# Performance work log

Measured on AMD Instinct MI355X. Metric: run time of the kernel, lower is better.

Reference implementation:

```python
import jax, jax.numpy as jnp
import numpy as np

N = 50000      # nodes
E = 800000     # edges
F_IN = 128     # input_dim
H = 4          # GAT heads
C = 32         # hidden_dim (per head)
HC = H * C     # 128, concat GAT output
NG = 64        # graphs in batch
OUT = 10       # classes


def _gat_conv(x, src, dst, W, att_src, att_dst, bias):
    # PyG GATConv (concat=True, add_self_loops=True, negative_slope=0.2)
    n = x.shape[0]
    h = (x @ W).reshape(n, H, -1)                      # [N,H,C]
    a_s = (h * att_src).sum(-1)                        # [N,H]
    a_d = (h * att_dst).sum(-1)                        # [N,H]
    loop = jnp.arange(n)
    s = jnp.concatenate([src, loop])                   # self-loops appended
    d = jnp.concatenate([dst, loop])
    e = jax.nn.leaky_relu(a_s[s] + a_d[d], 0.2)        # [E+N,H]
    m = jax.ops.segment_max(e, d, num_segments=n)
    e = jnp.exp(e - m[d])
    z = jax.ops.segment_sum(e, d, num_segments=n)
    alpha = e / (z[d] + 1e-16)                         # edge softmax per dst,head
    out = jax.ops.segment_sum(h[s] * alpha[..., None], d, num_segments=n)
    return out.reshape(n, -1) + bias                   # [N,H*C]


def setup_inputs() -> dict:
    key = jax.random.key(0)
    ks = jax.random.split(key, 20)
    g = lambda k, shp, fan: jax.random.normal(k, shp, jnp.float32) / np.sqrt(fan)
    inp = {
        'x': jax.random.normal(ks[0], (N, F_IN), jnp.float32),
        'edge_index': jax.random.randint(ks[1], (2, E), 0, N),
        'batch': jnp.sort(jax.random.randint(ks[2], (N,), 0, NG)),
        # GATConv 1: F_IN -> H*C
        'W1': g(ks[3], (F_IN, HC), F_IN),
        'as1': g(ks[4], (H, C), C), 'ad1': g(ks[5], (H, C), C),
        'b1': jnp.zeros((HC,), jnp.float32),
        # GATConv 2: H*C -> H*C
        'W2': g(ks[6], (HC, HC), HC),
        'as2': g(ks[7], (H, C), C), 'ad2': g(ks[8], (H, C), C),
        'b2': jnp.zeros((HC,), jnp.float32),
        # GraphConv: H*C -> C  (lin_rel has bias, lin_root does not)
        'W3r': g(ks[9], (HC, C), HC), 'W3l': g(ks[10], (HC, C), HC),
        'b3': jnp.zeros((C,), jnp.float32),
        # SAGEConv: C -> C (mean aggr; lin_l has bias, lin_r does not)
        'W4l': g(ks[11], (C, C), C), 'b4l': jnp.zeros((C,), jnp.float32),
        'W4r': g(ks[12], (C, C), C),
        # MLP head
        'Wf1': g(ks[13], (C, C), C), 'bf1': jnp.zeros((C,), jnp.float32),
        'Wf2': g(ks[14], (C, OUT), C), 'bf2': jnp.zeros((OUT,), jnp.float32),
    }
    return inp


def reference(x, edge_index, batch, W1, as1, ad1, b1, W2, as2, ad2, b2,
              W3r, W3l, b3, W4l, b4l, W4r, Wf1, bf1, Wf2, bf2):
    src, dst = edge_index[0], edge_index[1]
    relu = jax.nn.relu
    n = x.shape[0]
    # GAT layers (dropout is identity in eval)
    x = relu(_gat_conv(x, src, dst, W1, as1, ad1, b1))
    x = relu(_gat_conv(x, src, dst, W2, as2, ad2, b2))
    # GraphConv: lin_rel(sum_neighbors) + lin_root(x)
    agg = jax.ops.segment_sum(x[src], dst, num_segments=n)
    x = relu(agg @ W3r + b3 + x @ W3l)
    # SAGEConv: lin_l(mean_neighbors) + lin_r(x)
    deg = jax.ops.segment_sum(jnp.ones((src.shape[0],), x.dtype), dst, num_segments=n)
    mean = jax.ops.segment_sum(x[src], dst, num_segments=n) / jnp.maximum(deg, 1.0)[:, None]
    x = relu(mean @ W4l + b4l + x @ W4r)
    # global mean pool over graphs
    cnt = jax.ops.segment_sum(jnp.ones((n,), x.dtype), batch, num_segments=NG)
    gpool = jax.ops.segment_sum(x, batch, num_segments=NG) / jnp.maximum(cnt, 1.0)[:, None]
    gpool = relu(gpool @ Wf1 + bf1)
    return gpool @ Wf2 + bf2
```

## Files before the change

kernel.cpp:

```cpp
#include <hip/hip_runtime.h>
#include <hip/hip_bf16.h>
#include <type_traits>


typedef __bf16 v8bf __attribute__((ext_vector_type(8)));
typedef float  v4f  __attribute__((ext_vector_type(4)));

__device__ __forceinline__ float lrelu(float x) { return x > 0.f ? x : 0.2f * x; }

__device__ __forceinline__ float bf2f(__hip_bfloat16 b) {
    unsigned short u = *(const unsigned short*)&b;
    return __uint_as_float((unsigned)u << 16);
}
__device__ __forceinline__ unsigned short f2bf(float f) {
    unsigned u = __float_as_uint(f);
    unsigned r = (u + 0x7FFF + ((u >> 16) & 1)) >> 16;
    return (unsigned short)r;
}
__device__ __forceinline__ float bflo(int v) { return __uint_as_float((unsigned)v << 16); }
__device__ __forceinline__ float bfhi(int v) { return __uint_as_float((unsigned)v & 0xffff0000u); }
__device__ __forceinline__ int packbf2(float a, float b) {
    return (int)f2bf(a) | ((int)f2bf(b) << 16);
}


__global__ __launch_bounds__(256) void bucket_hist(const int* __restrict__ dst,
                                                   int* __restrict__ bcount,
                                                   int E, int nbuck) {
    __shared__ int hist[256];
    int t = threadIdx.x;
    for (int i = t; i < nbuck; i += 256) hist[i] = 0;
    __syncthreads();
    int base = blockIdx.x * 4096;
    #pragma unroll
    for (int k = 0; k < 16; ++k) {
        int e = base + k * 256 + t;
        if (e < E) atomicAdd(&hist[dst[e] >> 8], 1);
    }
    __syncthreads();
    for (int i = t; i < nbuck; i += 256) {
        int c = hist[i];
        if (c) atomicAdd(&bcount[i], c);
    }
}

__global__ __launch_bounds__(256) void scan_buckets(const int* __restrict__ bcount,
                                                    int* __restrict__ bbase,
                                                    int* __restrict__ gcursor,
                                                    int nbuck, int E,
                                                    int* __restrict__ rowptr, int n) {
    __shared__ int red[256];
    int t = threadIdx.x;
    int v = (t < nbuck) ? bcount[t] : 0;
    red[t] = v;
    __syncthreads();
    for (int off = 1; off < 256; off <<= 1) {
        int u = (t >= off) ? red[t - off] : 0;
        __syncthreads();
        red[t] += u;
        __syncthreads();
    }
    int ex = red[t] - v;
    if (t < nbuck) { bbase[t] = ex; gcursor[t] = ex; }
    if (t == 0) { bbase[nbuck] = E; rowptr[n] = E; }
}

__global__ __launch_bounds__(256) void bucket_scatter(const int* __restrict__ dst,
                                                      const int* __restrict__ src,
                                                      int* __restrict__ gcursor,
                                                      int* __restrict__ pairs,
                                                      int E, int nbuck) {
    __shared__ int hist[256], lcur[256];
    int t = threadIdx.x;
    for (int i = t; i < nbuck; i += 256) hist[i] = 0;
    __syncthreads();
    int base = blockIdx.x * 2048;
    int dreg[8];
    #pragma unroll
    for (int k = 0; k < 8; ++k) {
        int e = base + k * 256 + t;
        int d = (e < E) ? dst[e] : -1;
        dreg[k] = d;
        if (d >= 0) atomicAdd(&hist[d >> 8], 1);
    }
    __syncthreads();
    for (int i = t; i < nbuck; i += 256) {
        int c = hist[i];
        lcur[i] = c ? atomicAdd(&gcursor[i], c) : 0;
    }
    __syncthreads();
    #pragma unroll
    for (int k = 0; k < 8; ++k) {
        int e = base + k * 256 + t;
        if (e < E) {
            int d = dreg[k];
            int p = atomicAdd(&lcur[d >> 8], 1);
            pairs[p] = ((d & 255) << 17) | src[e];
        }
    }
}

__global__ __launch_bounds__(256) void bucket_fill(const int* __restrict__ pairs,
                                                   const int* __restrict__ bbase,
                                                   int* __restrict__ rowptr,
                                                   int* __restrict__ colsrc, int n) {
    __shared__ int deg[256], excl[256], cur[256];
    int b = blockIdx.x, t = threadIdx.x;
    int e0 = bbase[b], e1 = bbase[b + 1];
    int d0 = b << 8;
    deg[t] = 0;
    __syncthreads();
    for (int j = e0 + t; j < e1; j += 256)
        atomicAdd(&deg[pairs[j] >> 17], 1);
    __syncthreads();
    int v = deg[t];
    excl[t] = v;
    __syncthreads();
    for (int off = 1; off < 256; off <<= 1) {
        int u = (t >= off) ? excl[t - off] : 0;
        __syncthreads();
        excl[t] += u;
        __syncthreads();
    }
    int base = e0 + excl[t] - v;
    if (d0 + t < n) rowptr[d0 + t] = base;
    cur[t] = base;
    __syncthreads();
    for (int j = e0 + t; j < e1; j += 256) {
        int w = pairs[j];
        int p = atomicAdd(&cur[w >> 17], 1);
        colsrc[p] = w & 0x1FFFF;
    }
}

__global__ void convert_weights(const float* __restrict__ W1, const float* __restrict__ W2,
                                const float* __restrict__ W3r, const float* __restrict__ W3l,
                                __hip_bfloat16* __restrict__ W1t, __hip_bfloat16* __restrict__ W2t,
                                __hip_bfloat16* __restrict__ W3rt, __hip_bfloat16* __restrict__ W3lt) {
    int i = blockIdx.x * 256 + threadIdx.x;
    if (i < 16384) {
        int k = i >> 7, c = i & 127;
        *(unsigned short*)&W1t[c * 128 + k] = f2bf(W1[i]);
        *(unsigned short*)&W2t[c * 128 + k] = f2bf(W2[i]);
    }
    if (i < 4096) {
        int k = i >> 5, c = i & 31;
        *(unsigned short*)&W3rt[c * 128 + k] = f2bf(W3r[i]);
        *(unsigned short*)&W3lt[c * 128 + k] = f2bf(W3l[i]);
    }
}

template <typename T>
__global__ __launch_bounds__(256) void gemm_att_mfma(
    const T* __restrict__ X, const __hip_bfloat16* __restrict__ Wt,
    const float* __restrict__ att_s, const float* __restrict__ att_d,
    __hip_bfloat16* __restrict__ h, float* __restrict__ a_s, float* __restrict__ a_d, int n)
{
    __shared__ __align__(16) __hip_bfloat16 sWt[128 * 136];
    int t = threadIdx.x;
    for (int i = t; i < 128 * 16; i += 256) {
        int row = i >> 4, ch = i & 15;
        *(int4*)&sWt[row * 136 + ch * 8] = *(const int4*)&Wt[row * 128 + ch * 8];
    }
    __syncthreads();
    int wave = t >> 6, lane = t & 63, quad = lane >> 4, l16 = lane & 15;
    int rowbase = (blockIdx.x * 4 + wave) * 16;
    if (rowbase >= n) return;

    v8bf z;
    #pragma unroll
    for (int i = 0; i < 8; ++i) z[i] = (__bf16)0.f;
    int arow = rowbase + l16;
    bool ok = arow < n;
    v8bf af[4];
    if constexpr (std::is_same<T, float>::value) {
        const float* xf = X + (size_t)(ok ? arow : 0) * 128;
        #pragma unroll
        for (int ks = 0; ks < 4; ++ks) {
            if (ok) {
                float4 u = *(const float4*)&xf[ks * 32 + quad * 8];
                float4 v = *(const float4*)&xf[ks * 32 + quad * 8 + 4];
                v8bf a;
                unsigned short r;
                r = f2bf(u.x); a[0] = *(__bf16*)&r;
                r = f2bf(u.y); a[1] = *(__bf16*)&r;
                r = f2bf(u.z); a[2] = *(__bf16*)&r;
                r = f2bf(u.w); a[3] = *(__bf16*)&r;
                r = f2bf(v.x); a[4] = *(__bf16*)&r;
                r = f2bf(v.y); a[5] = *(__bf16*)&r;
                r = f2bf(v.z); a[6] = *(__bf16*)&r;
                r = f2bf(v.w); a[7] = *(__bf16*)&r;
                af[ks] = a;
            } else af[ks] = z;
        }
    } else {
        const v8bf* px = (const v8bf*)(X + (size_t)(ok ? arow : 0) * 128);
        #pragma unroll
        for (int ks = 0; ks < 4; ++ks) af[ks] = ok ? px[ks * 4 + quad] : z;
    }

    v4f acc[8];
    #pragma unroll
    for (int ct = 0; ct < 8; ++ct) acc[ct] = (v4f){0.f, 0.f, 0.f, 0.f};
    #pragma unroll
    for (int ct = 0; ct < 8; ++ct) {
        #pragma unroll
        for (int ks = 0; ks < 4; ++ks) {
            v8bf b = *(const v8bf*)&sWt[(ct * 16 + l16) * 136 + ks * 32 + quad * 8];
            acc[ct] = __builtin_amdgcn_mfma_f32_16x16x32_bf16(af[ks], b, acc[ct], 0, 0, 0);
        }
    }

    float sas[4][4], sad[4][4];
    #pragma unroll
    for (int r = 0; r < 4; ++r)
        #pragma unroll
        for (int hd = 0; hd < 4; ++hd) { sas[r][hd] = 0.f; sad[r][hd] = 0.f; }
    #pragma unroll
    for (int ct = 0; ct < 8; ++ct) {
        float sa = att_s[ct * 16 + l16];
        float da = att_d[ct * 16 + l16];
        int hd = ct >> 1;
        #pragma unroll
        for (int r = 0; r < 4; ++r) {
            float v = acc[ct][r];
            sas[r][hd] += v * sa;
            sad[r][hd] += v * da;
        }
    }
    #pragma unroll
    for (int reg = 0; reg < 4; ++reg) {
        int r = rowbase + quad * 4 + reg;
        if (r < n) {
            #pragma unroll
            for (int ct = 0; ct < 8; ++ct)
                *(unsigned short*)&h[(size_t)r * 128 + ct * 16 + l16] = f2bf(acc[ct][reg]);
        }
    }
    #pragma unroll
    for (int off = 1; off < 16; off <<= 1) {
        #pragma unroll
        for (int r = 0; r < 4; ++r)
            #pragma unroll
            for (int hd = 0; hd < 4; ++hd) {
                sas[r][hd] += __shfl_xor(sas[r][hd], off);
                sad[r][hd] += __shfl_xor(sad[r][hd], off);
            }
    }
    if (l16 == 0) {
        #pragma unroll
        for (int reg = 0; reg < 4; ++reg) {
            int r = rowbase + quad * 4 + reg;
            if (r < n) {
                float4 vs = {sas[reg][0], sas[reg][1], sas[reg][2], sas[reg][3]};
                float4 vd = {sad[reg][0], sad[reg][1], sad[reg][2], sad[reg][3]};
                *(float4*)&a_s[r * 4] = vs;
                *(float4*)&a_d[r * 4] = vd;
            }
        }
    }
}

__global__ __launch_bounds__(256) void gat_aggr(
    const __hip_bfloat16* __restrict__ h, const float* __restrict__ a_s,
    const float* __restrict__ a_d,
    const int* __restrict__ rowptr, const int* __restrict__ colsrc,
    const float* __restrict__ bias, __hip_bfloat16* __restrict__ out, int n)
{
    __shared__ float s_w[4][64 * 4];
    int t = threadIdx.x;
    int wave = t >> 6, lane = t & 63;
    int d = blockIdx.x * 4 + wave;
    if (d >= n) d = n - 1;
    int beg = rowptr[d], end = rowptr[d + 1];
    int cnt = end - beg;
    float4 ad4 = *(const float4*)&a_d[d * 4];
    float4 asd = *(const float4*)&a_s[d * 4];
    float es0 = lrelu(asd.x + ad4.x), es1 = lrelu(asd.y + ad4.y);
    float es2 = lrelu(asd.z + ad4.z), es3 = lrelu(asd.w + ad4.w);
    float z0 = 0.f, z1 = 0.f, z2 = 0.f, z3 = 0.f;

    int l16 = lane & 15, egrp = lane >> 4;
    int ch = l16 * 8;
    int head = l16 >> 2;
    float acc[8];
    #pragma unroll
    for (int i = 0; i < 8; ++i) acc[i] = 0.f;

    for (int j0 = 0; j0 < cnt; j0 += 64) {
        int ne = min(64, cnt - j0);
        float w0 = 0.f, w1 = 0.f, w2 = 0.f, w3 = 0.f;
        int s = 0;
        if (lane < ne) {
            s = colsrc[beg + j0 + lane];
            float4 sv = *(const float4*)&a_s[s * 4];
            w0 = __expf(lrelu(sv.x + ad4.x));
            w1 = __expf(lrelu(sv.y + ad4.y));
            w2 = __expf(lrelu(sv.z + ad4.z));
            w3 = __expf(lrelu(sv.w + ad4.w));
        }
        z0 += w0; z1 += w1; z2 += w2; z3 += w3;
        float4 wv = {w0, w1, w2, w3};
        *(float4*)&s_w[wave][lane * 4] = wv;
        __asm volatile("s_waitcnt lgkmcnt(0)" ::: "memory");
        int kmax = (ne + 3) >> 2;
        for (int k = 0; k < kmax; ++k) {
            int j = egrp + 4 * k;
            int ss = __shfl(s, min(j, 63));
            if (j < ne) {
                float wj = s_w[wave][j * 4 + head];
                int4 u = *(const int4*)&h[(size_t)ss * 128 + ch];
                acc[0] += wj * bflo(u.x); acc[1] += wj * bfhi(u.x);
                acc[2] += wj * bflo(u.y); acc[3] += wj * bfhi(u.y);
                acc[4] += wj * bflo(u.z); acc[5] += wj * bfhi(u.z);
                acc[6] += wj * bflo(u.w); acc[7] += wj * bfhi(u.w);
            }
        }
    }
    #pragma unroll
    for (int off = 1; off < 64; off <<= 1) {
        z0 += __shfl_xor(z0, off);
        z1 += __shfl_xor(z1, off);
        z2 += __shfl_xor(z2, off);
        z3 += __shfl_xor(z3, off);
    }
    #pragma unroll
    for (int off = 16; off < 64; off <<= 1)
        #pragma unroll
        for (int i = 0; i < 8; ++i) acc[i] += __shfl_xor(acc[i], off);

    if (egrp == 0) {
        float zh = (head < 2) ? (head == 0 ? z0 : z1) : (head == 2 ? z2 : z3);
        float eh = (head < 2) ? (head == 0 ? es0 : es1) : (head == 2 ? es2 : es3);
        float ws = __expf(eh);
        float inv = 1.f / (zh + ws + 1e-16f);
        int4 hu = *(const int4*)&h[(size_t)d * 128 + ch];
        float hs[8] = {bflo(hu.x), bfhi(hu.x), bflo(hu.y), bfhi(hu.y),
                       bflo(hu.z), bfhi(hu.z), bflo(hu.w), bfhi(hu.w)};
        float4 b0 = *(const float4*)&bias[ch];
        float4 b1 = *(const float4*)&bias[ch + 4];
        float o[8];
        o[0] = fmaxf((acc[0] + ws * hs[0]) * inv + b0.x, 0.f);
        o[1] = fmaxf((acc[1] + ws * hs[1]) * inv + b0.y, 0.f);
        o[2] = fmaxf((acc[2] + ws * hs[2]) * inv + b0.z, 0.f);
        o[3] = fmaxf((acc[3] + ws * hs[3]) * inv + b0.w, 0.f);
        o[4] = fmaxf((acc[4] + ws * hs[4]) * inv + b1.x, 0.f);
        o[5] = fmaxf((acc[5] + ws * hs[5]) * inv + b1.y, 0.f);
        o[6] = fmaxf((acc[6] + ws * hs[6]) * inv + b1.z, 0.f);
        o[7] = fmaxf((acc[7] + ws * hs[7]) * inv + b1.w, 0.f);
        int4 ou;
        ou.x = packbf2(o[0], o[1]); ou.y = packbf2(o[2], o[3]);
        ou.z = packbf2(o[4], o[5]); ou.w = packbf2(o[6], o[7]);
        *(int4*)&out[(size_t)d * 128 + ch] = ou;
    }
}

__global__ __launch_bounds__(256) void graphconv_lin(
    const __hip_bfloat16* __restrict__ Xb,
    const __hip_bfloat16* __restrict__ Wrt, const __hip_bfloat16* __restrict__ Wlt,
    const float* __restrict__ bias, __hip_bfloat16* __restrict__ y,
    float* __restrict__ root, int n)
{
    __shared__ __align__(16) __hip_bfloat16 sWr[32 * 136], sWl[32 * 136];
    int t = threadIdx.x;
    for (int i = t; i < 32 * 16; i += 256) {
        int row = i >> 4, ch = i & 15;
        *(int4*)&sWr[row * 136 + ch * 8] = *(const int4*)&Wrt[row * 128 + ch * 8];
        *(int4*)&sWl[row * 136 + ch * 8] = *(const int4*)&Wlt[row * 128 + ch * 8];
    }
    __syncthreads();
    int wave = t >> 6, lane = t & 63, quad = lane >> 4, l16 = lane & 15;
    int rowbase = (blockIdx.x * 4 + wave) * 16;
    if (rowbase >= n) return;

    v8bf z;
    #pragma unroll
    for (int i = 0; i < 8; ++i) z[i] = (__bf16)0.f;
    int arow = rowbase + l16;
    bool ok = arow < n;
    const v8bf* px = (const v8bf*)(Xb + (size_t)(ok ? arow : 0) * 128);
    v8bf fx[4];
    #pragma unroll
    for (int ks = 0; ks < 4; ++ks) fx[ks] = ok ? px[ks * 4 + quad] : z;

    v4f accR[2], accL[2];
    #pragma unroll
    for (int ct = 0; ct < 2; ++ct) {
        accR[ct] = (v4f){0.f, 0.f, 0.f, 0.f};
        accL[ct] = (v4f){0.f, 0.f, 0.f, 0.f};
        #pragma unroll
        for (int ks = 0; ks < 4; ++ks) {
            v8bf br = *(const v8bf*)&sWr[(ct * 16 + l16) * 136 + ks * 32 + quad * 8];
            accR[ct] = __builtin_amdgcn_mfma_f32_16x16x32_bf16(fx[ks], br, accR[ct], 0, 0, 0);
            v8bf bl = *(const v8bf*)&sWl[(ct * 16 + l16) * 136 + ks * 32 + quad * 8];
            accL[ct] = __builtin_amdgcn_mfma_f32_16x16x32_bf16(fx[ks], bl, accL[ct], 0, 0, 0);
        }
    }
    #pragma unroll
    for (int ct = 0; ct < 2; ++ct) {
        float bcol = bias[ct * 16 + l16];
        #pragma unroll
        for (int reg = 0; reg < 4; ++reg) {
            int r = rowbase + quad * 4 + reg;
            if (r < n) {
                *(unsigned short*)&y[(size_t)r * 32 + ct * 16 + l16] = f2bf(accR[ct][reg]);
                root[(size_t)r * 32 + ct * 16 + l16] = accL[ct][reg] + bcol;
            }
        }
    }
}

__global__ __launch_bounds__(256) void graphconv_aggr(
    const __hip_bfloat16* __restrict__ y, const float* __restrict__ root,
    const int* __restrict__ rowptr, const int* __restrict__ colsrc,
    __hip_bfloat16* __restrict__ x3, int n)
{
    int t = threadIdx.x;
    int wave = t >> 6, lane = t & 63;
    int d = blockIdx.x * 4 + wave;
    if (d >= n) d = n - 1;
    int beg = rowptr[d], end = rowptr[d + 1];
    int cnt = end - beg;
    int l4 = lane & 3, egrp = lane >> 2;
    int ch = l4 * 8;
    float acc[8];
    #pragma unroll
    for (int i = 0; i < 8; ++i) acc[i] = 0.f;
    for (int j0 = 0; j0 < cnt; j0 += 64) {
        int ne = min(64, cnt - j0);
        int s = (lane < ne) ? colsrc[beg + j0 + lane] : 0;
        int kmax = (ne + 15) >> 4;
        for (int k = 0; k < kmax; ++k) {
            int j = egrp + 16 * k;
            int ss = __shfl(s, min(j, 63));
            if (j < ne) {
                int4 u = *(const int4*)&y[(size_t)ss * 32 + ch];
                acc[0] += bflo(u.x); acc[1] += bfhi(u.x);
                acc[2] += bflo(u.y); acc[3] += bfhi(u.y);
                acc[4] += bflo(u.z); acc[5] += bfhi(u.z);
                acc[6] += bflo(u.w); acc[7] += bfhi(u.w);
            }
        }
    }
    #pragma unroll
    for (int off = 4; off < 64; off <<= 1)
        #pragma unroll
        for (int i = 0; i < 8; ++i) acc[i] += __shfl_xor(acc[i], off);
    if (egrp == 0) {
        float4 r0 = *(const float4*)&root[(size_t)d * 32 + ch];
        float4 r1 = *(const float4*)&root[(size_t)d * 32 + ch + 4];
        float o[8];
        o[0] = fmaxf(acc[0] + r0.x, 0.f); o[1] = fmaxf(acc[1] + r0.y, 0.f);
        o[2] = fmaxf(acc[2] + r0.z, 0.f); o[3] = fmaxf(acc[3] + r0.w, 0.f);
        o[4] = fmaxf(acc[4] + r1.x, 0.f); o[5] = fmaxf(acc[5] + r1.y, 0.f);
        o[6] = fmaxf(acc[6] + r1.z, 0.f); o[7] = fmaxf(acc[7] + r1.w, 0.f);
        int4 ou;
        ou.x = packbf2(o[0], o[1]); ou.y = packbf2(o[2], o[3]);
        ou.z = packbf2(o[4], o[5]); ou.w = packbf2(o[6], o[7]);
        *(int4*)&x3[(size_t)d * 32 + ch] = ou;
    }
}

__global__ __launch_bounds__(256) void mean_aggr32(
    const __hip_bfloat16* __restrict__ x, const int* __restrict__ rowptr,
    const int* __restrict__ colsrc, float* __restrict__ mean, int n)
{
    int t = threadIdx.x;
    int wave = t >> 6, lane = t & 63;
    int d = blockIdx.x * 4 + wave;
    if (d >= n) d = n - 1;
    int beg = rowptr[d], end = rowptr[d + 1];
    int cnt = end - beg;
    int l4 = lane & 3, egrp = lane >> 2;
    int ch = l4 * 8;
    float acc[8];
    #pragma unroll
    for (int i = 0; i < 8; ++i) acc[i] = 0.f;
    for (int j0 = 0; j0 < cnt; j0 += 64) {
        int ne = min(64, cnt - j0);
        int s = (lane < ne) ? colsrc[beg + j0 + lane] : 0;
        int kmax = (ne + 15) >> 4;
        for (int k = 0; k < kmax; ++k) {
            int j = egrp + 16 * k;
            int ss = __shfl(s, min(j, 63));
            if (j < ne) {
                int4 u = *(const int4*)&x[(size_t)ss * 32 + ch];
                acc[0] += bflo(u.x); acc[1] += bfhi(u.x);
                acc[2] += bflo(u.y); acc[3] += bfhi(u.y);
                acc[4] += bflo(u.z); acc[5] += bfhi(u.z);
                acc[6] += bflo(u.w); acc[7] += bfhi(u.w);
            }
        }
    }
    #pragma unroll
    for (int off = 4; off < 64; off <<= 1)
        #pragma unroll
        for (int i = 0; i < 8; ++i) acc[i] += __shfl_xor(acc[i], off);
    if (egrp == 0) {
        float invd = 1.f / fmaxf((float)cnt, 1.f);
        float4 lo = {acc[0] * invd, acc[1] * invd, acc[2] * invd, acc[3] * invd};
        float4 hi = {acc[4] * invd, acc[5] * invd, acc[6] * invd, acc[7] * invd};
        *(float4*)&mean[(size_t)d * 32 + ch]     = lo;
        *(float4*)&mean[(size_t)d * 32 + ch + 4] = hi;
    }
}

__global__ __launch_bounds__(256) void sage_gemm(
    const float* __restrict__ mean, const __hip_bfloat16* __restrict__ xin,
    const float* __restrict__ Wl, const float* __restrict__ bl,
    const float* __restrict__ Wr, float* __restrict__ out, int n)
{
    __shared__ __align__(16) float sWl[32 * 32], sWr[32 * 32];
    __shared__ __align__(16) float sm[8 * 32], sx[8 * 32];
    int t = threadIdx.x;
    for (int i = t; i < 1024; i += 256) { sWl[i] = Wl[i]; sWr[i] = Wr[i]; }
    int c = t & 31, rr = t >> 5;
    float bc = bl[c];
    for (int row0 = blockIdx.x * 8; row0 < n; row0 += gridDim.x * 8) {
        __syncthreads();
        {
            int i = t;
            int r = i >> 5, cc = i & 31;
            int row = row0 + r;
            sm[i] = (row < n) ? mean[row * 32 + cc] : 0.f;
            sx[i] = (row < n) ? bf2f(xin[row * 32 + cc]) : 0.f;
        }
        __syncthreads();
        float acc = bc;
        const float4* pm = (const float4*)&sm[rr * 32];
        const float4* px = (const float4*)&sx[rr * 32];
        #pragma unroll
        for (int k4 = 0; k4 < 8; ++k4) {
            float4 vm = pm[k4], vx = px[k4];
            const float* wl = &sWl[(k4 * 4) * 32 + c];
            const float* wr = &sWr[(k4 * 4) * 32 + c];
            acc += vm.x * wl[0] + vm.y * wl[32] + vm.z * wl[64] + vm.w * wl[96];
            acc += vx.x * wr[0] + vx.y * wr[32] + vx.z * wr[64] + vx.w * wr[96];
        }
        int row = row0 + rr;
        if (row < n) out[row * 32 + c] = fmaxf(acc, 0.f);
    }
}

__device__ __forceinline__ int lower_bound_i(const int* a, int n, int key) {
    int lo = 0, hi = n;
    while (lo < hi) { int mid = (lo + hi) >> 1; if (a[mid] < key) lo = mid + 1; else hi = mid; }
    return lo;
}

__global__ __launch_bounds__(256) void pool_kernel(
    const float* __restrict__ x, const int* __restrict__ batch,
    float* __restrict__ gpool, int n)
{
    int g = blockIdx.x;
    int lo = lower_bound_i(batch, n, g);
    int hi = lower_bound_i(batch, n, g + 1);
    int t = threadIdx.x;
    int c = t & 31, rr = t >> 5;
    float acc = 0.f;
    for (int i = lo + rr; i < hi; i += 8) acc += x[i * 32 + c];
    __shared__ float sred[256];
    sred[t] = acc;
    __syncthreads();
    if (t < 128) sred[t] += sred[t + 128];
    __syncthreads();
    if (t < 64) sred[t] += sred[t + 64];
    __syncthreads();
    if (t < 32) {
        float v = sred[t] + sred[t + 32];
        gpool[g * 32 + t] = v / fmaxf((float)(hi - lo), 1.f);
    }
}

__global__ __launch_bounds__(256) void head_kernel(
    const float* __restrict__ gpool, const float* __restrict__ Wf1, const float* __restrict__ bf1,
    const float* __restrict__ Wf2, const float* __restrict__ bf2, float* __restrict__ out)
{
    __shared__ float sg[64 * 32], st[64 * 32];
    __shared__ float sW1[32 * 32], sW2[32 * 10];
    int t = threadIdx.x;
    for (int i = t; i < 2048; i += 256) sg[i] = gpool[i];
    for (int i = t; i < 1024; i += 256) sW1[i] = Wf1[i];
    for (int i = t; i < 320; i += 256) sW2[i] = Wf2[i];
    __syncthreads();
    for (int i = t; i < 2048; i += 256) {
        int g = i >> 5, c = i & 31;
        float acc = bf1[c];
        #pragma unroll
        for (int k = 0; k < 32; ++k) acc += sg[g * 32 + k] * sW1[k * 32 + c];
        st[i] = fmaxf(acc, 0.f);
    }
    __syncthreads();
    for (int i = t; i < 640; i += 256) {
        int g = i / 10, o = i - g * 10;
        float acc = bf2[o];
        #pragma unroll
        for (int k = 0; k < 32; ++k) acc += st[g * 32 + k] * sW2[k * 10 + o];
        out[i] = acc;
    }
}

extern "C" void kernel_launch(void* const* d_in, const int* in_sizes, int n_in,
                              void* d_out, int out_size, void* d_ws, size_t ws_size,
                              hipStream_t stream) {
    const float* x    = (const float*)d_in[0];
    const int*   ei   = (const int*)d_in[1];
    const int*   batch= (const int*)d_in[2];
    const float* W1   = (const float*)d_in[3];
    const float* as1  = (const float*)d_in[4];
    const float* ad1  = (const float*)d_in[5];
    const float* b1   = (const float*)d_in[6];
    const float* W2   = (const float*)d_in[7];
    const float* as2  = (const float*)d_in[8];
    const float* ad2  = (const float*)d_in[9];
    const float* b2   = (const float*)d_in[10];
    const float* W3r  = (const float*)d_in[11];
    const float* W3l  = (const float*)d_in[12];
    const float* b3   = (const float*)d_in[13];
    const float* W4l  = (const float*)d_in[14];
    const float* b4l  = (const float*)d_in[15];
    const float* W4r  = (const float*)d_in[16];
    const float* Wf1  = (const float*)d_in[17];
    const float* bf1  = (const float*)d_in[18];
    const float* Wf2  = (const float*)d_in[19];
    const float* bf2  = (const float*)d_in[20];

    const int N = in_sizes[0] / 128;
    const int E = in_sizes[1] / 2;
    const int* src = ei;
    const int* dst = ei + E;

    char* p = (char*)d_ws;
    auto alloc = [&](size_t bytes) -> void* {
        void* r = (void*)p;
        p += (bytes + 255) & ~(size_t)255;
        return r;
    };
    __hip_bfloat16* buf1 = (__hip_bfloat16*)alloc((size_t)N * 128 * 2);
    __hip_bfloat16* buf2 = (__hip_bfloat16*)alloc((size_t)N * 128 * 2);
    __hip_bfloat16* buf3 = (__hip_bfloat16*)alloc((size_t)N * 128 * 2);
    float* aS     = (float*)alloc((size_t)N * 4 * 4);
    float* aD     = (float*)alloc((size_t)N * 4 * 4);
    int*   rowptr = (int*)alloc((size_t)(N + 1) * 4);
    int*   colsrc = (int*)alloc((size_t)E * 4);
    int*   bcount = (int*)alloc(256 * 4);
    int*   bbase  = (int*)alloc(257 * 4);
    int*   gcursor= (int*)alloc(256 * 4);
    __hip_bfloat16* W1t  = (__hip_bfloat16*)alloc(128 * 128 * 2);
    __hip_bfloat16* W2t  = (__hip_bfloat16*)alloc(128 * 128 * 2);
    __hip_bfloat16* W3rt = (__hip_bfloat16*)alloc(32 * 128 * 2);
    __hip_bfloat16* W3lt = (__hip_bfloat16*)alloc(32 * 128 * 2);
    float* gpool  = (float*)alloc(64 * 32 * 4);

    __hip_bfloat16* X3b  = buf2;
    float*          MEAN = (float*)((char*)buf2 + (((size_t)N * 32 * 2 + 255) & ~(size_t)255));
    float*          X4   = (float*)buf1;
    __hip_bfloat16* Y32  = buf3;
    float*          ROOT = (float*)((char*)buf3 + (((size_t)N * 32 * 2 + 255) & ~(size_t)255));
    int*            pairs = (int*)buf3;

    const int nbuck = (N + 255) >> 8;

    hipMemsetAsync(bcount, 0, 256 * 4, stream);
    bucket_hist<<<(E + 4095) / 4096, 256, 0, stream>>>(dst, bcount, E, nbuck);
    scan_buckets<<<1, 256, 0, stream>>>(bcount, bbase, gcursor, nbuck, E, rowptr, N);
    bucket_scatter<<<(E + 2047) / 2048, 256, 0, stream>>>(dst, src, gcursor, pairs, E, nbuck);
    bucket_fill<<<nbuck, 256, 0, stream>>>(pairs, bbase, rowptr, colsrc, N);

    convert_weights<<<64, 256, 0, stream>>>(W1, W2, W3r, W3l, W1t, W2t, W3rt, W3lt);

    const int gmm = (N + 63) / 64;
    const int gag = (N + 3) / 4;
    gemm_att_mfma<float><<<gmm, 256, 0, stream>>>(x, W1t, as1, ad1, buf3, aS, aD, N);
    gat_aggr<<<gag, 256, 0, stream>>>(buf3, aS, aD, rowptr, colsrc, b1, buf2, N);
    gemm_att_mfma<__hip_bfloat16><<<gmm, 256, 0, stream>>>(buf2, W2t, as2, ad2, buf3, aS, aD, N);
    gat_aggr<<<gag, 256, 0, stream>>>(buf3, aS, aD, rowptr, colsrc, b2, buf1, N);
    graphconv_lin<<<gmm, 256, 0, stream>>>(buf1, W3rt, W3lt, b3, Y32, ROOT, N);
    graphconv_aggr<<<gag, 256, 0, stream>>>(Y32, ROOT, rowptr, colsrc, X3b, N);
    mean_aggr32<<<gag, 256, 0, stream>>>(X3b, rowptr, colsrc, MEAN, N);
    sage_gemm<<<1024, 256, 0, stream>>>(MEAN, X3b, W4l, b4l, W4r, X4, N);
    pool_kernel<<<64, 256, 0, stream>>>(X4, batch, gpool, N);
    head_kernel<<<1, 256, 0, stream>>>(gpool, Wf1, bf1, Wf2, bf2, (float*)d_out);
}
```

Measured before the change: 361.1 us.

## Fold attention vectors into GEMM weights and merge weight conversion into scan

Precomputes W·att_src and W·att_dst per head and appends them, split into bf16 hi/lo pairs, as 16 extra rows of the transposed weight matrix. The GEMM then gets the attention logits from one extra MFMA column tile instead of a per-row reduction with shuffles. Weight conversion is merged into the bucket scan kernel to save a launch, and the gather loops drop their per-edge branch in favour of masking plus unroll by two. It adds 12.5% more MFMA work and 16 more shared rows, and changes logit rounding to bf16 inputs with an fp32 hi/lo split.

```diff
diff --git a/kernel.cpp b/kernel.cpp
--- a/kernel.cpp
+++ b/kernel.cpp
@@ -8,15 +8,14 @@
 
 __device__ __forceinline__ float lrelu(float x) { return x > 0.f ? x : 0.2f * x; }
 
-__device__ __forceinline__ float bf2f(__hip_bfloat16 b) {
-    unsigned short u = *(const unsigned short*)&b;
-    return __uint_as_float((unsigned)u << 16);
-}
 __device__ __forceinline__ unsigned short f2bf(float f) {
     unsigned u = __float_as_uint(f);
     unsigned r = (u + 0x7FFF + ((u >> 16) & 1)) >> 16;
     return (unsigned short)r;
 }
+__device__ __forceinline__ float bfbits2f(unsigned short u) {
+    return __uint_as_float((unsigned)u << 16);
+}
 __device__ __forceinline__ float bflo(int v) { return __uint_as_float((unsigned)v << 16); }
 __device__ __forceinline__ float bfhi(int v) { return __uint_as_float((unsigned)v & 0xffff0000u); }
 __device__ __forceinline__ int packbf2(float a, float b) {
@@ -44,25 +43,68 @@
     }
 }
 
-__global__ __launch_bounds__(256) void scan_buckets(const int* __restrict__ bcount,
-                                                    int* __restrict__ bbase,
-                                                    int* __restrict__ gcursor,
-                                                    int nbuck, int E,
-                                                    int* __restrict__ rowptr, int n) {
-    __shared__ int red[256];
-    int t = threadIdx.x;
-    int v = (t < nbuck) ? bcount[t] : 0;
-    red[t] = v;
-    __syncthreads();
-    for (int off = 1; off < 256; off <<= 1) {
-        int u = (t >= off) ? red[t - off] : 0;
+__global__ __launch_bounds__(256) void scan_convert(
+    const int* __restrict__ bcount, int* __restrict__ bbase, int* __restrict__ gcursor,
+    int nbuck, int E, int* __restrict__ rowptr, int n,
+    const float* __restrict__ W1, const float* __restrict__ W2,
+    const float* __restrict__ W3r, const float* __restrict__ W3l,
+    const float* __restrict__ as1, const float* __restrict__ ad1,
+    const float* __restrict__ as2, const float* __restrict__ ad2,
+    __hip_bfloat16* __restrict__ W1t, __hip_bfloat16* __restrict__ W2t,
+    __hip_bfloat16* __restrict__ W3rt, __hip_bfloat16* __restrict__ W3lt)
+{
+    int t = threadIdx.x;
+    if (blockIdx.x == 0) {
+        __shared__ int red[256];
+        int v = (t < nbuck) ? bcount[t] : 0;
+        red[t] = v;
         __syncthreads();
-        red[t] += u;
-        __syncthreads();
-    }
-    int ex = red[t] - v;
-    if (t < nbuck) { bbase[t] = ex; gcursor[t] = ex; }
-    if (t == 0) { bbase[nbuck] = E; rowptr[n] = E; }
+        for (int off = 1; off < 256; off <<= 1) {
+            int u = (t >= off) ? red[t - off] : 0;
+            __syncthreads();
+            red[t] += u;
+            __syncthreads();
+        }
+        int ex = red[t] - v;
+        if (t < nbuck) { bbase[t] = ex; gcursor[t] = ex; }
+        if (t == 0) { bbase[nbuck] = E; rowptr[n] = E; }
+        return;
+    }
+    int b = blockIdx.x - 1;
+    int i = b * 256 + t;
+    {
+        int k = i >> 7, c = i & 127;
+        *(unsigned short*)&W1t[c * 128 + k] = f2bf(W1[i]);
+        *(unsigned short*)&W2t[c * 128 + k] = f2bf(W2[i]);
+    }
+    if (i < 4096) {
+        int k = i >> 5, c = i & 31;
+        *(unsigned short*)&W3rt[c * 128 + k] = f2bf(W3r[i]);
+        *(unsigned short*)&W3lt[c * 128 + k] = f2bf(W3l[i]);
+    }
+    if (b == 0) {
+        for (int u = t; u < 512; u += 256) {
+            int k = u & 127, hd = u >> 7;
+            float vs1 = 0.f, vd1 = 0.f, vs2 = 0.f, vd2 = 0.f;
+            #pragma unroll
+            for (int j = 0; j < 32; ++j) {
+                int c = hd * 32 + j;
+                float w1 = W1[k * 128 + c], w2 = W2[k * 128 + c];
+                vs1 += w1 * as1[c]; vd1 += w1 * ad1[c];
+                vs2 += w2 * as2[c]; vd2 += w2 * ad2[c];
+            }
+            unsigned short h1s = f2bf(vs1), h1d = f2bf(vd1);
+            unsigned short h2s = f2bf(vs2), h2d = f2bf(vd2);
+            *(unsigned short*)&W1t[(128 + hd) * 128 + k] = h1s;
+            *(unsigned short*)&W1t[(132 + hd) * 128 + k] = f2bf(vs1 - bfbits2f(h1s));
+            *(unsigned short*)&W1t[(136 + hd) * 128 + k] = h1d;
+            *(unsigned short*)&W1t[(140 + hd) * 128 + k] = f2bf(vd1 - bfbits2f(h1d));
+            *(unsigned short*)&W2t[(128 + hd) * 128 + k] = h2s;
+            *(unsigned short*)&W2t[(132 + hd) * 128 + k] = f2bf(vs2 - bfbits2f(h2s));
+            *(unsigned short*)&W2t[(136 + hd) * 128 + k] = h2d;
+            *(unsigned short*)&W2t[(140 + hd) * 128 + k] = f2bf(vd2 - bfbits2f(h2d));
+        }
+    }
 }
 
 __global__ __launch_bounds__(256) void bucket_scatter(const int* __restrict__ dst,
@@ -133,32 +175,14 @@
     }
 }
 
-__global__ void convert_weights(const float* __restrict__ W1, const float* __restrict__ W2,
-                                const float* __restrict__ W3r, const float* __restrict__ W3l,
-                                __hip_bfloat16* __restrict__ W1t, __hip_bfloat16* __restrict__ W2t,
-                                __hip_bfloat16* __restrict__ W3rt, __hip_bfloat16* __restrict__ W3lt) {
-    int i = blockIdx.x * 256 + threadIdx.x;
-    if (i < 16384) {
-        int k = i >> 7, c = i & 127;
-        *(unsigned short*)&W1t[c * 128 + k] = f2bf(W1[i]);
-        *(unsigned short*)&W2t[c * 128 + k] = f2bf(W2[i]);
-    }
-    if (i < 4096) {
-        int k = i >> 5, c = i & 31;
-        *(unsigned short*)&W3rt[c * 128 + k] = f2bf(W3r[i]);
-        *(unsigned short*)&W3lt[c * 128 + k] = f2bf(W3l[i]);
-    }
-}
-
 template <typename T>
 __global__ __launch_bounds__(256) void gemm_att_mfma(
     const T* __restrict__ X, const __hip_bfloat16* __restrict__ Wt,
-    const float* __restrict__ att_s, const float* __restrict__ att_d,
     __hip_bfloat16* __restrict__ h, float* __restrict__ a_s, float* __restrict__ a_d, int n)
 {
-    __shared__ __align__(16) __hip_bfloat16 sWt[128 * 136];
-    int t = threadIdx.x;
-    for (int i = t; i < 128 * 16; i += 256) {
+    __shared__ __align__(16) __hip_bfloat16 sWt[144 * 136];
+    int t = threadIdx.x;
+    for (int i = t; i < 144 * 16; i += 256) {
         int row = i >> 4, ch = i & 15;
         *(int4*)&sWt[row * 136 + ch * 8] = *(const int4*)&Wt[row * 128 + ch * 8];
     }
@@ -199,11 +223,11 @@
         for (int ks = 0; ks < 4; ++ks) af[ks] = ok ? px[ks * 4 + quad] : z;
     }
 
-    v4f acc[8];
-    #pragma unroll
-    for (int ct = 0; ct < 8; ++ct) acc[ct] = (v4f){0.f, 0.f, 0.f, 0.f};
-    #pragma unroll
-    for (int ct = 0; ct < 8; ++ct) {
+    v4f acc[9];
+    #pragma unroll
+    for (int ct = 0; ct < 9; ++ct) acc[ct] = (v4f){0.f, 0.f, 0.f, 0.f};
+    #pragma unroll
+    for (int ct = 0; ct < 9; ++ct) {
         #pragma unroll
         for (int ks = 0; ks < 4; ++ks) {
             v8bf b = *(const v8bf*)&sWt[(ct * 16 + l16) * 136 + ks * 32 + quad * 8];
@@ -211,23 +235,6 @@
         }
     }
 
-    float sas[4][4], sad[4][4];
-    #pragma unroll
-    for (int r = 0; r < 4; ++r)
-        #pragma unroll
-        for (int hd = 0; hd < 4; ++hd) { sas[r][hd] = 0.f; sad[r][hd] = 0.f; }
-    #pragma unroll
-    for (int ct = 0; ct < 8; ++ct) {
-        float sa = att_s[ct * 16 + l16];
-        float da = att_d[ct * 16 + l16];
-        int hd = ct >> 1;
-        #pragma unroll
-        for (int r = 0; r < 4; ++r) {
-            float v = acc[ct][r];
-            sas[r][hd] += v * sa;
-            sad[r][hd] += v * da;
-        }
-    }
     #pragma unroll
     for (int reg = 0; reg < 4; ++reg) {
         int r = rowbase + quad * 4 + reg;
@@ -238,25 +245,12 @@
         }
     }
     #pragma unroll
-    for (int off = 1; off < 16; off <<= 1) {
-        #pragma unroll
-        for (int r = 0; r < 4; ++r)
-            #pragma unroll
-            for (int hd = 0; hd < 4; ++hd) {
-                sas[r][hd] += __shfl_xor(sas[r][hd], off);
-                sad[r][hd] += __shfl_xor(sad[r][hd], off);
-            }
-    }
-    if (l16 == 0) {
-        #pragma unroll
-        for (int reg = 0; reg < 4; ++reg) {
-            int r = rowbase + quad * 4 + reg;
-            if (r < n) {
-                float4 vs = {sas[reg][0], sas[reg][1], sas[reg][2], sas[reg][3]};
-                float4 vd = {sad[reg][0], sad[reg][1], sad[reg][2], sad[reg][3]};
-                *(float4*)&a_s[r * 4] = vs;
-                *(float4*)&a_d[r * 4] = vd;
-            }
+    for (int reg = 0; reg < 4; ++reg) {
+        float v = acc[8][reg] + __shfl_xor(acc[8][reg], 4);
+        int r = rowbase + quad * 4 + reg;
+        if (r < n) {
+            if (l16 < 4)                    a_s[r * 4 + l16] = v;
+            else if (l16 >= 8 && l16 < 12)  a_d[r * 4 + (l16 - 8)] = v;
         }
     }
 }
@@ -304,17 +298,16 @@
         *(float4*)&s_w[wave][lane * 4] = wv;
         __asm volatile("s_waitcnt lgkmcnt(0)" ::: "memory");
         int kmax = (ne + 3) >> 2;
+        #pragma unroll 2
         for (int k = 0; k < kmax; ++k) {
             int j = egrp + 4 * k;
-            int ss = __shfl(s, min(j, 63));
-            if (j < ne) {
-                float wj = s_w[wave][j * 4 + head];
-                int4 u = *(const int4*)&h[(size_t)ss * 128 + ch];
-                acc[0] += wj * bflo(u.x); acc[1] += wj * bfhi(u.x);
-                acc[2] += wj * bflo(u.y); acc[3] += wj * bfhi(u.y);
-                acc[4] += wj * bflo(u.z); acc[5] += wj * bfhi(u.z);
-                acc[6] += wj * bflo(u.w); acc[7] += wj * bfhi(u.w);
-            }
+            int ss = __shfl(s, j);
+            float wj = s_w[wave][j * 4 + head];
+            int4 u = *(const int4*)&h[(size_t)ss * 128 + ch];
+            acc[0] += wj * bflo(u.x); acc[1] += wj * bfhi(u.x);
+            acc[2] += wj * bflo(u.y); acc[3] += wj * bfhi(u.y);
+            acc[4] += wj * bflo(u.z); acc[5] += wj * bfhi(u.z);
+            acc[6] += wj * bflo(u.w); acc[7] += wj * bfhi(u.w);
         }
     }
     #pragma unroll
@@ -430,16 +423,16 @@
         int ne = min(64, cnt - j0);
         int s = (lane < ne) ? colsrc[beg + j0 + lane] : 0;
         int kmax = (ne + 15) >> 4;
+        #pragma unroll 2
         for (int k = 0; k < kmax; ++k) {
             int j = egrp + 16 * k;
-            int ss = __shfl(s, min(j, 63));
-            if (j < ne) {
-                int4 u = *(const int4*)&y[(size_t)ss * 32 + ch];
-                acc[0] += bflo(u.x); acc[1] += bfhi(u.x);
-                acc[2] += bflo(u.y); acc[3] += bfhi(u.y);
-                acc[4] += bflo(u.z); acc[5] += bfhi(u.z);
-                acc[6] += bflo(u.w); acc[7] += bfhi(u.w);
-            }
+            int ss = __shfl(s, j);
+            float m = (j < ne) ? 1.f : 0.f;
+            int4 u = *(const int4*)&y[(size_t)ss * 32 + ch];
+            acc[0] += m * bflo(u.x); acc[1] += m * bfhi(u.x);
+            acc[2] += m * bflo(u.y); acc[3] += m * bfhi(u.y);
+            acc[4] += m * bflo(u.z); acc[5] += m * bfhi(u.z);
+            acc[6] += m * bflo(u.w); acc[7] += m * bfhi(u.w);
         }
     }
     #pragma unroll
@@ -480,16 +473,16 @@
         int ne = min(64, cnt - j0);
         int s = (lane < ne) ? colsrc[beg + j0 + lane] : 0;
         int kmax = (ne + 15) >> 4;
+        #pragma unroll 2
         for (int k = 0; k < kmax; ++k) {
             int j = egrp + 16 * k;
-            int ss = __shfl(s, min(j, 63));
-            if (j < ne) {
-                int4 u = *(const int4*)&x[(size_t)ss * 32 + ch];
-                acc[0] += bflo(u.x); acc[1] += bfhi(u.x);
-                acc[2] += bflo(u.y); acc[3] += bfhi(u.y);
-                acc[4] += bflo(u.z); acc[5] += bfhi(u.z);
-                acc[6] += bflo(u.w); acc[7] += bfhi(u.w);
-            }
+            int ss = __shfl(s, j);
+            float m = (j < ne) ? 1.f : 0.f;
+            int4 u = *(const int4*)&x[(size_t)ss * 32 + ch];
+            acc[0] += m * bflo(u.x); acc[1] += m * bfhi(u.x);
+            acc[2] += m * bflo(u.y); acc[3] += m * bfhi(u.y);
+            acc[4] += m * bflo(u.z); acc[5] += m * bfhi(u.z);
+            acc[6] += m * bflo(u.w); acc[7] += m * bfhi(u.w);
         }
     }
     #pragma unroll
@@ -523,7 +516,7 @@
             int r = i >> 5, cc = i & 31;
             int row = row0 + r;
             sm[i] = (row < n) ? mean[row * 32 + cc] : 0.f;
-            sx[i] = (row < n) ? bf2f(xin[row * 32 + cc]) : 0.f;
+            sx[i] = (row < n) ? bfbits2f(*(const unsigned short*)&xin[row * 32 + cc]) : 0.f;
         }
         __syncthreads();
         float acc = bc;
@@ -646,8 +639,8 @@
     int*   bcount = (int*)alloc(256 * 4);
     int*   bbase  = (int*)alloc(257 * 4);
     int*   gcursor= (int*)alloc(256 * 4);
-    __hip_bfloat16* W1t  = (__hip_bfloat16*)alloc(128 * 128 * 2);
-    __hip_bfloat16* W2t  = (__hip_bfloat16*)alloc(128 * 128 * 2);
+    __hip_bfloat16* W1t  = (__hip_bfloat16*)alloc(144 * 128 * 2);
+    __hip_bfloat16* W2t  = (__hip_bfloat16*)alloc(144 * 128 * 2);
     __hip_bfloat16* W3rt = (__hip_bfloat16*)alloc(32 * 128 * 2);
     __hip_bfloat16* W3lt = (__hip_bfloat16*)alloc(32 * 128 * 2);
     float* gpool  = (float*)alloc(64 * 32 * 4);
@@ -663,17 +656,17 @@
 
     hipMemsetAsync(bcount, 0, 256 * 4, stream);
     bucket_hist<<<(E + 4095) / 4096, 256, 0, stream>>>(dst, bcount, E, nbuck);
-    scan_buckets<<<1, 256, 0, stream>>>(bcount, bbase, gcursor, nbuck, E, rowptr, N);
+    scan_convert<<<65, 256, 0, stream>>>(bcount, bbase, gcursor, nbuck, E, rowptr, N,
+                                         W1, W2, W3r, W3l, as1, ad1, as2, ad2,
+                                         W1t, W2t, W3rt, W3lt);
     bucket_scatter<<<(E + 2047) / 2048, 256, 0, stream>>>(dst, src, gcursor, pairs, E, nbuck);
     bucket_fill<<<nbuck, 256, 0, stream>>>(pairs, bbase, rowptr, colsrc, N);
 
-    convert_weights<<<64, 256, 0, stream>>>(W1, W2, W3r, W3l, W1t, W2t, W3rt, W3lt);
-
     const int gmm = (N + 63) / 64;
     const int gag = (N + 3) / 4;
-    gemm_att_mfma<float><<<gmm, 256, 0, stream>>>(x, W1t, as1, ad1, buf3, aS, aD, N);
+    gemm_att_mfma<float><<<gmm, 256, 0, stream>>>(x, W1t, buf3, aS, aD, N);
     gat_aggr<<<gag, 256, 0, stream>>>(buf3, aS, aD, rowptr, colsrc, b1, buf2, N);
-    gemm_att_mfma<__hip_bfloat16><<<gmm, 256, 0, stream>>>(buf2, W2t, as2, ad2, buf3, aS, aD, N);
+    gemm_att_mfma<__hip_bfloat16><<<gmm, 256, 0, stream>>>(buf2, W2t, buf3, aS, aD, N);
     gat_aggr<<<gag, 256, 0, stream>>>(buf3, aS, aD, rowptr, colsrc, b2, buf1, N);
     graphconv_lin<<<gmm, 256, 0, stream>>>(buf1, W3rt, W3lt, b3, Y32, ROOT, N);
     graphconv_aggr<<<gag, 256, 0, stream>>>(Y32, ROOT, rowptr, colsrc, X3b, N);
```

Measured after the change: 357.4 us. About the same (-1.0%).
